# Kernel optimization log

Measured on AMD Instinct MI355X. Metric: run time of the kernel, lower is better.

## Reference

```python
import jax, jax.numpy as jnp
import numpy as np

B, E, S = 64, 256, 32        # batch, projection_size (=MHA embed dim), seq_l
H = 16                        # MHA heads
D_FINAL = 10                  # label space
K_CLASSES = D_FINAL * (D_FINAL - 1) // 2 + 1  # 46, header output dim
N_PATIENTS = 8
P_PAIRS = N_PATIENTS * (B // N_PATIENTS) ** 2  # 512 same-patient pairs (static)


def _pair_lookup(D):
    # class id of sorted label pair: (0,0)->0, then (a,b) a<b in lexicographic
    # order, matching torch.unique(rows of triu meshgrid) ordering.
    lut = np.zeros((D, D), np.int32)
    idx = 1
    for a in range(D):
        for b in range(a + 1, D):
            lut[a, b] = idx
            lut[b, a] = idx
            idx += 1
    return lut


def setup_inputs():
    ks = jax.random.split(jax.random.key(0), 10)
    s = 1.0 / np.sqrt(E)
    return {
        "features": jax.random.normal(ks[0], (B, E, S), jnp.float32),
        "labels0": jax.random.randint(ks[1], (B,), 0, D_FINAL, jnp.int32),
        "labels1": (jnp.arange(B, dtype=jnp.int32) // (B // N_PATIENTS)),
        "in_proj_w": jax.random.normal(ks[2], (3 * E, E), jnp.float32) * s,
        "in_proj_b": jax.random.normal(ks[3], (3 * E,), jnp.float32) * 0.01,
        "out_proj_w": jax.random.normal(ks[4], (E, E), jnp.float32) * s,
        "out_proj_b": jax.random.normal(ks[5], (E,), jnp.float32) * 0.01,
        "final_w": jax.random.normal(ks[6], (1, S), jnp.float32) * (1.0 / np.sqrt(S)),
        "final_b": jax.random.normal(ks[7], (1,), jnp.float32) * 0.01,
        "header_w": jax.random.normal(ks[8], (K_CLASSES, E), jnp.float32) * s,
        "header_b": jax.random.normal(ks[9], (K_CLASSES,), jnp.float32) * 0.01,
    }


def reference(features, labels0, labels1, in_proj_w, in_proj_b, out_proj_w,
              out_proj_b, final_w, final_b, header_w, header_b):
    # ---- pair selection: (i, j) with same patient id (labels1) ----
    mask = (labels1[:, None] == labels1[None, :]).reshape(-1)  # (B*B,)
    sel = jnp.nonzero(mask, size=P_PAIRS, fill_value=0)[0]      # row-major order
    valid = (jnp.arange(P_PAIRS) < mask.sum()).astype(jnp.float32)
    i_idx, j_idx = sel // B, sel % B                            # (P,), (P,)

    # ---- pair class labels: sorted (l_i, l_j), equal labels -> (0, 0) ----
    a, b = labels0[i_idx], labels0[j_idx]
    eq = a == b
    lo = jnp.where(eq, 0, jnp.minimum(a, b))
    hi = jnp.where(eq, 0, jnp.maximum(a, b))
    lut = jnp.asarray(_pair_lookup(D_FINAL))
    y = lut[lo, hi]                                             # (P,) class ids

    # ---- gather pair features; torch permutes to (2, P, seq_l, C) ----
    q_in = jnp.transpose(features[i_idx], (0, 2, 1))  # (P, S, E) query
    kv_in = jnp.transpose(features[j_idx], (0, 2, 1))  # (P, S, E) key/value

    # ---- MultiheadAttention (eval, dropout off); L = pair axis P, N = S ----
    Wq, Wk, Wv = jnp.split(in_proj_w, 3, axis=0)
    bq, bk, bv = jnp.split(in_proj_b, 3, axis=0)
    hd = E // H
    q = (q_in @ Wq.T + bq).reshape(P_PAIRS, S, H, hd)
    k = (kv_in @ Wk.T + bk).reshape(P_PAIRS, S, H, hd)
    v = (kv_in @ Wv.T + bv).reshape(P_PAIRS, S, H, hd)
    scores = jnp.einsum('lshd,mshd->shlm', q, k) / np.sqrt(hd)  # (S,H,P,P)
    attn = jax.nn.softmax(scores, axis=-1)
    o = jnp.einsum('shlm,mshd->lshd', attn, v).reshape(P_PAIRS, S, E)
    o = o @ out_proj_w.T + out_proj_b                           # (P, S, E)

    # ---- backbone.final: Linear over the seq axis (S -> 1), squeeze ----
    h = jnp.einsum('pse,s->pe', o, final_w[0]) + final_b[0]     # (P, E)
    logits = h @ header_w.T + header_b                          # (P, K)

    # ---- inverse-frequency class weights over selected pairs ----
    counts = jnp.zeros(K_CLASSES, jnp.float32).at[y].add(valid)
    w = jnp.where(counts > 0, 1.0 / jnp.maximum(counts, 1.0), 0.0)

    # ---- weighted cross-entropy (torch semantics: / sum of weights) ----
    nll = -jax.nn.log_softmax(logits, axis=-1)[jnp.arange(P_PAIRS), y]
    wy = w[y] * valid
    loss = jnp.sum(wy * nll) / jnp.sum(wy)
    return loss
```

## Files before the change

### kernel.cpp

```cpp
#include <hip/hip_runtime.h>
#include <math.h>

#define B_ 64
#define E_ 256
#define S_ 32
#define H_ 16
#define P_ 512
#define KC_ 46
#define QKV_N (B_*S_*E_)

#define WS_CM     0
#define WS_WK     256
#define WS_INVDEN 3328
#define WS_C      3392
#define WS_M      3584
#define WS_WT     16384
#define WS_QKV    262144
#define WS_OPART  1835008

__global__ __launch_bounds__(256) void k_prep(
    const float* __restrict__ w, const int* __restrict__ labels0,
    const int* __restrict__ labels1, const float* __restrict__ wout,
    const float* __restrict__ bout, const float* __restrict__ fw,
    const float* __restrict__ fbi, const float* __restrict__ hw,
    const float* __restrict__ hb, float* __restrict__ ws,
    float* __restrict__ out) {
  __shared__ float sm[8192];
  const int bid = blockIdx.x, t = threadIdx.x;
  if (bid < 48) {
    const int r0 = (bid >> 2) * 64, c0 = (bid & 3) * 64;
    float* ts = sm;
#pragma unroll
    for (int p = 0; p < 4; ++p) {
      int r = p*16 + (t >> 4), c4 = t & 15;
      float4 v = *(const float4*)(w + (size_t)(r0+r)*E_ + c0 + c4*4);
      ts[(c4*4+0)*65 + r] = v.x;
      ts[(c4*4+1)*65 + r] = v.y;
      ts[(c4*4+2)*65 + r] = v.z;
      ts[(c4*4+3)*65 + r] = v.w;
    }
    __syncthreads();
    float* WT = ws + WS_WT;
#pragma unroll
    for (int p = 0; p < 4; ++p) {
      int c = p*16 + (t >> 4), r4 = t & 15;
      float4 v = make_float4(ts[c*65 + r4*4], ts[c*65 + r4*4 + 1],
                             ts[c*65 + r4*4 + 2], ts[c*65 + r4*4 + 3]);
      *(float4*)(WT + (size_t)(c0+c)*768 + r0 + r4*4) = v;
    }
  } else if (bid == 48) {
    float* csh = sm;
    float* cls = sm + 64;
    float* wsh = sm + 112;
    float* den = sm + 160;
    float* Wk  = sm + 192;
    int* scan = (int*)(sm + 3200);
    int* l0   = (int*)(sm + 3456);
    int* l1   = (int*)(sm + 3520);
    int* seli = (int*)(sm + 3584);
    int* selj = (int*)(sm + 4096);
    if (t < 64) { l0[t] = labels0[t]; l1[t] = labels1[t]; csh[t] = 0.f; }
    if (t < KC_) cls[t] = 0.f;
    if (t == 0) den[0] = 0.f;
    for (int i = t; i < 2944; i += 256) Wk[i] = 0.f;
    __syncthreads();
    unsigned bits = 0; int c = 0;
    for (int u = 0; u < 16; ++u) {
      int idx = t*16 + u;
      if (l1[idx>>6] == l1[idx&63]) { bits |= 1u<<u; ++c; }
    }
    scan[t] = c; __syncthreads();
    for (int off = 1; off < 256; off <<= 1) {
      int v = (t >= off) ? scan[t-off] : 0;
      __syncthreads();
      scan[t] += v;
      __syncthreads();
    }
    const int total = scan[255];
    int rank = scan[t] - c;
    for (int p = t; p < P_; p += 256)
      if (p >= total) { seli[p] = 0; selj[p] = 0; }
    for (int u = 0; u < 16; ++u) {
      if (bits & (1u<<u)) {
        if (rank < P_) { int idx = t*16+u; seli[rank] = idx>>6; selj[rank] = idx&63; }
        ++rank;
      }
    }
    __syncthreads();
    int ii[2], yy[2]; float vv[2];
#pragma unroll
    for (int r = 0; r < 2; ++r) {
      int p = t + r*256;
      int i = seli[p], j = selj[p];
      atomicAdd(&csh[j], 1.0f);
      int la = l0[i], lb = l0[j];
      int y;
      if (la == lb) y = 0;
      else {
        int lo = la < lb ? la : lb, hi = la < lb ? lb : la;
        y = 1 + lo*9 - (lo*(lo-1))/2 + (hi-lo-1);
      }
      float v = (p < total) ? 1.f : 0.f;
      if (v > 0.f) atomicAdd(&cls[y], 1.f);
      ii[r] = i; yy[r] = y; vv[r] = v;
    }
    __syncthreads();
    if (t < KC_) {
      float cv = cls[t];
      wsh[t] = cv > 0.f ? 1.0f/cv : 0.f;
      if (cv > 0.f) atomicAdd(den, 1.0f);
    }
    __syncthreads();
#pragma unroll
    for (int r = 0; r < 2; ++r)
      if (vv[r] > 0.f) atomicAdd(&Wk[ii[r]*KC_ + yy[r]], wsh[yy[r]]);
    __syncthreads();
    if (t < 64) ws[WS_CM + t] = csh[t];
    for (int i = t; i < 2944; i += 256) ws[WS_WK + i] = Wk[i];
    if (t == 0) ws[WS_INVDEN] = 1.0f / den[0];
  } else if (bid < 95) {
    int k = bid - 49;
    float* hwsh = sm;
    float* redA = sm + 256;
    float* redB = sm + 512;
    hwsh[t] = hw[k*E_ + t];
    __syncthreads();
    float a0 = 0.f;
#pragma unroll 8
    for (int e = 0; e < E_; ++e) a0 = fmaf(hwsh[e], wout[e*E_ + t], a0);
    ws[WS_M + k*E_ + t] = a0;
    redA[t] = hwsh[t];
    redB[t] = hwsh[t]*bout[t];
    __syncthreads();
    for (int off = 128; off > 0; off >>= 1) {
      if (t < off) { redA[t] += redA[t+off]; redB[t] += redB[t+off]; }
      __syncthreads();
    }
    if (t == 0) {
      float sfw = 0.f;
      for (int s = 0; s < S_; ++s) sfw += fw[s];
      ws[WS_C + k] = fbi[0]*redA[0] + sfw*redB[0] + hb[k];
    }
  } else {
    if (t == 0) out[0] = 0.f;
  }
}

__global__ __launch_bounds__(256) void k_proj(
    const float* __restrict__ feat, const float* __restrict__ bias,
    float* __restrict__ ws) {
  const int cc = blockIdx.x, b = blockIdx.y, t = threadIdx.x;
  __shared__ float xs[E_*S_];
  float4* xs4 = (float4*)xs;
  const float4* fb4 = (const float4*)(feat + (size_t)b*(E_*S_));
#pragma unroll
  for (int i = 0; i < 8; ++i) xs4[i*256 + t] = fb4[i*256 + t];
  __syncthreads();
  const int to = t & 31, ts = t >> 5;
  const float4* WT4 = (const float4*)(ws + WS_WT);
  const int wi = cc*32 + to;
  float acc[4][4];
#pragma unroll
  for (int o = 0; o < 4; ++o)
#pragma unroll
    for (int si = 0; si < 4; ++si) acc[o][si] = 0.f;
#pragma unroll 4
  for (int e = 0; e < E_; ++e) {
    float4 wv4 = WT4[e*192 + wi];
    float4 x4  = xs4[e*8 + ts];
    float wv[4] = {wv4.x, wv4.y, wv4.z, wv4.w};
    float xv[4] = {x4.x, x4.y, x4.z, x4.w};
#pragma unroll
    for (int o = 0; o < 4; ++o)
#pragma unroll
      for (int si = 0; si < 4; ++si)
        acc[o][si] = fmaf(wv[o], xv[si], acc[o][si]);
  }
  const int out0 = cc*128 + to*4;
  float4 bb = *(const float4*)(bias + out0);
  const int r = out0 >> 8, e_in = out0 & 255;
  float* dst = ws + WS_QKV + (size_t)r*QKV_N + (size_t)b*(S_*E_) + e_in;
#pragma unroll
  for (int si = 0; si < 4; ++si) {
    int s = ts*4 + si;
    *(float4*)(dst + s*E_) = make_float4(acc[0][si]+bb.x, acc[1][si]+bb.y,
                                         acc[2][si]+bb.z, acc[3][si]+bb.w);
  }
}

__global__ __launch_bounds__(256) void k_attn(
    float* __restrict__ ws, const float* __restrict__ fw) {
  const int s = blockIdx.x >> 4, h = blockIdx.x & 15;
  const int t = threadIdx.x;
  __shared__ float qT[16*68], kT[16*68], vs[64*20];
  __shared__ float sc[64*68], pT[64*68], red[4*64*20], cm[64];
  const float* qkv = ws + WS_QKV;
  const int a = t >> 2, dq = t & 3;
  {
    size_t off = (size_t)a*(S_*E_) + (size_t)s*E_ + h*16 + dq*4;
    float4 q4 = *(const float4*)(qkv + off);
    float4 k4 = *(const float4*)(qkv + QKV_N + off);
    float4 v4 = *(const float4*)(qkv + 2*(size_t)QKV_N + off);
    qT[(dq*4+0)*68 + a] = q4.x; qT[(dq*4+1)*68 + a] = q4.y;
    qT[(dq*4+2)*68 + a] = q4.z; qT[(dq*4+3)*68 + a] = q4.w;
    kT[(dq*4+0)*68 + a] = k4.x; kT[(dq*4+1)*68 + a] = k4.y;
    kT[(dq*4+2)*68 + a] = k4.z; kT[(dq*4+3)*68 + a] = k4.w;
    *(float4*)(vs + a*20 + dq*4) = v4;
  }
  if (t < 64) cm[t] = ws[WS_CM + t];
  __syncthreads();
  const int ta = t & 15, tb = t >> 4;
  float sa[4][4];
#pragma unroll
  for (int r = 0; r < 4; ++r)
#pragma unroll
    for (int c = 0; c < 4; ++c) sa[r][c] = 0.f;
#pragma unroll
  for (int d = 0; d < 16; ++d) {
    float4 qv = *(float4*)(qT + d*68 + ta*4);
    float4 kv = *(float4*)(kT + d*68 + tb*4);
    float qr[4] = {qv.x,qv.y,qv.z,qv.w};
    float kc[4] = {kv.x,kv.y,kv.z,kv.w};
#pragma unroll
    for (int r = 0; r < 4; ++r)
#pragma unroll
      for (int c = 0; c < 4; ++c) sa[r][c] = fmaf(qr[r], kc[c], sa[r][c]);
  }
#pragma unroll
  for (int r = 0; r < 4; ++r)
    *(float4*)(sc + (ta*4+r)*68 + tb*4) =
        make_float4(sa[r][0]*0.25f, sa[r][1]*0.25f, sa[r][2]*0.25f, sa[r][3]*0.25f);
  __syncthreads();
  float pv[16], cmv[16];
#pragma unroll
  for (int i4 = 0; i4 < 4; ++i4) {
    float4 v = *(float4*)(sc + a*68 + dq*16 + i4*4);
    pv[i4*4+0] = v.x; pv[i4*4+1] = v.y; pv[i4*4+2] = v.z; pv[i4*4+3] = v.w;
  }
#pragma unroll
  for (int i = 0; i < 16; ++i) cmv[i] = cm[dq*16 + i];
  float Mx = -1e30f;
#pragma unroll
  for (int i = 0; i < 16; ++i) if (cmv[i] > 0.f) Mx = fmaxf(Mx, pv[i]);
  Mx = fmaxf(Mx, __shfl_xor(Mx, 1));
  Mx = fmaxf(Mx, __shfl_xor(Mx, 2));
  float z = 0.f;
#pragma unroll
  for (int i = 0; i < 16; ++i) {
    float e = (cmv[i] > 0.f) ? cmv[i]*__expf(pv[i]-Mx) : 0.f;
    pv[i] = e; z += e;
  }
  z += __shfl_xor(z, 1);
  z += __shfl_xor(z, 2);
  float rz = 1.0f / z;
#pragma unroll
  for (int i = 0; i < 16; ++i) pT[(dq*16+i)*68 + a] = pv[i]*rz;
  __syncthreads();
  const int g = t >> 6, td = (t >> 4) & 3, ta2 = t & 15;
  float o[4][4];
#pragma unroll
  for (int r = 0; r < 4; ++r)
#pragma unroll
    for (int c = 0; c < 4; ++c) o[r][c] = 0.f;
#pragma unroll
  for (int i = 0; i < 16; ++i) {
    int bb = g*16 + i;
    float4 p4 = *(float4*)(pT + bb*68 + ta2*4);
    float4 v4 = *(float4*)(vs + bb*20 + td*4);
    float pr[4] = {p4.x,p4.y,p4.z,p4.w};
    float vc[4] = {v4.x,v4.y,v4.z,v4.w};
#pragma unroll
    for (int r = 0; r < 4; ++r)
#pragma unroll
      for (int c = 0; c < 4; ++c) o[r][c] = fmaf(pr[r], vc[c], o[r][c]);
  }
#pragma unroll
  for (int r = 0; r < 4; ++r)
    *(float4*)(red + g*1280 + (ta2*4+r)*20 + td*4) =
        make_float4(o[r][0], o[r][1], o[r][2], o[r][3]);
  __syncthreads();
  const float fwS = fw[s];
  float4 osum = make_float4(0.f, 0.f, 0.f, 0.f);
#pragma unroll
  for (int g2 = 0; g2 < 4; ++g2) {
    float4 v = *(float4*)(red + g2*1280 + a*20 + dq*4);
    osum.x += v.x; osum.y += v.y; osum.z += v.z; osum.w += v.w;
  }
  float* dst = ws + WS_OPART + (size_t)s*(H_*B_*16) + h*(B_*16) + a*16 + dq*4;
  *(float4*)dst = make_float4(fwS*osum.x, fwS*osum.y, fwS*osum.z, fwS*osum.w);
}

__global__ __launch_bounds__(256) void k_final(
    const float* __restrict__ ws, float* __restrict__ out) {
  const int aa = blockIdx.x, t = threadIdx.x;
  __shared__ float oh[256], lg[64];
  {
    const float* op = ws + WS_OPART + (t>>4)*(B_*16) + aa*16 + (t&15);
    float acc = 0.f;
#pragma unroll
    for (int s = 0; s < S_; ++s) acc += op[(size_t)s*(H_*B_*16)];
    oh[t] = acc;
  }
  __syncthreads();
  const int k = t >> 2, q = t & 3;
  if (k < KC_) {
    float lv = 0.f;
    const float4* M4 = (const float4*)(ws + WS_M + k*E_ + q*64);
    const float4* o4 = (const float4*)(oh + q*64);
#pragma unroll
    for (int j = 0; j < 16; ++j) {
      float4 m = M4[j], o = o4[j];
      lv = fmaf(m.x, o.x, lv); lv = fmaf(m.y, o.y, lv);
      lv = fmaf(m.z, o.z, lv); lv = fmaf(m.w, o.w, lv);
    }
    lv += __shfl_xor(lv, 1);
    lv += __shfl_xor(lv, 2);
    if (q == 0) lg[k] = lv + ws[WS_C + k];
  }
  __syncthreads();
  if (t < 64) {
    float x = (t < KC_) ? lg[t] : -1e30f;
    float Mx = x;
#pragma unroll
    for (int off = 1; off < 64; off <<= 1) Mx = fmaxf(Mx, __shfl_xor(Mx, off));
    float z = (t < KC_) ? __expf(x - Mx) : 0.f;
#pragma unroll
    for (int off = 1; off < 64; off <<= 1) z += __shfl_xor(z, off);
    float lse = Mx + __logf(z);
    float term = (t < KC_) ? ws[WS_WK + aa*KC_ + t] * (lse - x) : 0.f;
#pragma unroll
    for (int off = 1; off < 64; off <<= 1) term += __shfl_xor(term, off);
    if (t == 0) atomicAdd(out, term * ws[WS_INVDEN]);
  }
}

extern "C" void kernel_launch(void* const* d_in, const int* in_sizes, int n_in,
                              void* d_out, int out_size, void* d_ws, size_t ws_size,
                              hipStream_t stream) {
  const float* feat    = (const float*)d_in[0];
  const int*   labels0 = (const int*)d_in[1];
  const int*   labels1 = (const int*)d_in[2];
  const float* ipw     = (const float*)d_in[3];
  const float* ipb     = (const float*)d_in[4];
  const float* opw     = (const float*)d_in[5];
  const float* opb     = (const float*)d_in[6];
  const float* fw      = (const float*)d_in[7];
  const float* fbi     = (const float*)d_in[8];
  const float* hw      = (const float*)d_in[9];
  const float* hb      = (const float*)d_in[10];
  float* out = (float*)d_out;
  float* ws  = (float*)d_ws;

  k_prep<<<96, 256, 0, stream>>>(ipw, labels0, labels1, opw, opb, fw, fbi,
                                 hw, hb, ws, out);
  k_proj<<<dim3(6, 64), 256, 0, stream>>>(feat, ipb, ws);
  k_attn<<<512, 256, 0, stream>>>(ws, fw);
  k_final<<<64, 256, 0, stream>>>(ws, out);
}
```

Baseline: 126.9 us.

## Fuse all four stages into one cooperative kernel with grid-wide syncs

Replaces the four separate kernel launches (prep, projection, attention, final) with a single cooperative kernel of 512 blocks that separates stages with grid.sync(). The QKV projection is remapped so each block handles one batch row and 96 outputs, with each thread computing 12 outputs for one sequence position. The attention stage reuses the score buffer for probabilities and drops the cross-group reduction buffer by having each thread accumulate over all 64 keys. This removes launch gaps and inter-kernel drain, at the cost of grid-barrier overhead and a cooperative launch that requires all 512 blocks to be co-resident, with each block holding 32 KB of shared memory.

```diff
diff --git a/kernel.cpp b/kernel.cpp
--- a/kernel.cpp
+++ b/kernel.cpp
@@ -1,5 +1,8 @@
 #include <hip/hip_runtime.h>
+#include <hip/hip_cooperative_groups.h>
 #include <math.h>
+
+namespace cg = cooperative_groups;
 
 #define B_ 64
 #define E_ 256
@@ -18,22 +21,24 @@
 #define WS_QKV    262144
 #define WS_OPART  1835008
 
-__global__ __launch_bounds__(256) void k_prep(
-    const float* __restrict__ w, const int* __restrict__ labels0,
-    const int* __restrict__ labels1, const float* __restrict__ wout,
-    const float* __restrict__ bout, const float* __restrict__ fw,
+__global__ __launch_bounds__(256) void k_fused(
+    const float* __restrict__ feat, const int* __restrict__ labels0,
+    const int* __restrict__ labels1, const float* __restrict__ ipw,
+    const float* __restrict__ ipb, const float* __restrict__ opw,
+    const float* __restrict__ opb, const float* __restrict__ fw,
     const float* __restrict__ fbi, const float* __restrict__ hw,
-    const float* __restrict__ hb, float* __restrict__ ws,
-    float* __restrict__ out) {
+    const float* __restrict__ hb, float* ws, float* out) {
   __shared__ float sm[8192];
+  cg::grid_group grid = cg::this_grid();
   const int bid = blockIdx.x, t = threadIdx.x;
+
   if (bid < 48) {
     const int r0 = (bid >> 2) * 64, c0 = (bid & 3) * 64;
     float* ts = sm;
 #pragma unroll
     for (int p = 0; p < 4; ++p) {
       int r = p*16 + (t >> 4), c4 = t & 15;
-      float4 v = *(const float4*)(w + (size_t)(r0+r)*E_ + c0 + c4*4);
+      float4 v = *(const float4*)(ipw + (size_t)(r0+r)*E_ + c0 + c4*4);
       ts[(c4*4+0)*65 + r] = v.x;
       ts[(c4*4+1)*65 + r] = v.y;
       ts[(c4*4+2)*65 + r] = v.z;
@@ -127,10 +132,10 @@
     __syncthreads();
     float a0 = 0.f;
 #pragma unroll 8
-    for (int e = 0; e < E_; ++e) a0 = fmaf(hwsh[e], wout[e*E_ + t], a0);
+    for (int e = 0; e < E_; ++e) a0 = fmaf(hwsh[e], opw[e*E_ + t], a0);
     ws[WS_M + k*E_ + t] = a0;
     redA[t] = hwsh[t];
-    redB[t] = hwsh[t]*bout[t];
+    redB[t] = hwsh[t]*opb[t];
     __syncthreads();
     for (int off = 128; off > 0; off >>= 1) {
       if (t < off) { redA[t] += redA[t+off]; redB[t] += redB[t+off]; }
@@ -141,196 +146,192 @@
       for (int s = 0; s < S_; ++s) sfw += fw[s];
       ws[WS_C + k] = fbi[0]*redA[0] + sfw*redB[0] + hb[k];
     }
-  } else {
+  } else if (bid == 95) {
     if (t == 0) out[0] = 0.f;
   }
-}
-
-__global__ __launch_bounds__(256) void k_proj(
-    const float* __restrict__ feat, const float* __restrict__ bias,
-    float* __restrict__ ws) {
-  const int cc = blockIdx.x, b = blockIdx.y, t = threadIdx.x;
-  __shared__ float xs[E_*S_];
-  float4* xs4 = (float4*)xs;
-  const float4* fb4 = (const float4*)(feat + (size_t)b*(E_*S_));
-#pragma unroll
-  for (int i = 0; i < 8; ++i) xs4[i*256 + t] = fb4[i*256 + t];
-  __syncthreads();
-  const int to = t & 31, ts = t >> 5;
-  const float4* WT4 = (const float4*)(ws + WS_WT);
-  const int wi = cc*32 + to;
-  float acc[4][4];
-#pragma unroll
-  for (int o = 0; o < 4; ++o)
-#pragma unroll
-    for (int si = 0; si < 4; ++si) acc[o][si] = 0.f;
+  grid.sync();
+
+  {
+    const int b = bid >> 3, oc = bid & 7;
+    const float4* fb4 = (const float4*)(feat + (size_t)b*(E_*S_));
+    float4* xs4 = (float4*)sm;
+#pragma unroll
+    for (int i = 0; i < 8; ++i) xs4[i*256 + t] = fb4[i*256 + t];
+    __syncthreads();
+    const int s = t & 31, to8 = t >> 5;
+    const int out0 = oc*96 + to8*12;
+    const float4* WT4 = (const float4*)(ws + WS_WT);
+    const int wbase = out0 >> 2;
+    float acc[12];
+#pragma unroll
+    for (int i = 0; i < 12; ++i) acc[i] = 0.f;
 #pragma unroll 4
-  for (int e = 0; e < E_; ++e) {
-    float4 wv4 = WT4[e*192 + wi];
-    float4 x4  = xs4[e*8 + ts];
-    float wv[4] = {wv4.x, wv4.y, wv4.z, wv4.w};
-    float xv[4] = {x4.x, x4.y, x4.z, x4.w};
-#pragma unroll
-    for (int o = 0; o < 4; ++o)
-#pragma unroll
-      for (int si = 0; si < 4; ++si)
-        acc[o][si] = fmaf(wv[o], xv[si], acc[o][si]);
+    for (int e = 0; e < E_; ++e) {
+      float xv = sm[e*32 + s];
+      float4 w0 = WT4[e*192 + wbase];
+      float4 w1 = WT4[e*192 + wbase + 1];
+      float4 w2 = WT4[e*192 + wbase + 2];
+      acc[0] = fmaf(w0.x, xv, acc[0]);  acc[1] = fmaf(w0.y, xv, acc[1]);
+      acc[2] = fmaf(w0.z, xv, acc[2]);  acc[3] = fmaf(w0.w, xv, acc[3]);
+      acc[4] = fmaf(w1.x, xv, acc[4]);  acc[5] = fmaf(w1.y, xv, acc[5]);
+      acc[6] = fmaf(w1.z, xv, acc[6]);  acc[7] = fmaf(w1.w, xv, acc[7]);
+      acc[8] = fmaf(w2.x, xv, acc[8]);  acc[9] = fmaf(w2.y, xv, acc[9]);
+      acc[10] = fmaf(w2.z, xv, acc[10]); acc[11] = fmaf(w2.w, xv, acc[11]);
+    }
+#pragma unroll
+    for (int g = 0; g < 3; ++g) {
+      int og = out0 + g*4;
+      float4 bb = *(const float4*)(ipb + og);
+      int r = og >> 8, e_in = og & 255;
+      float* dst = ws + WS_QKV + (size_t)r*QKV_N + (size_t)b*(S_*E_) + s*E_ + e_in;
+      *(float4*)dst = make_float4(acc[g*4+0]+bb.x, acc[g*4+1]+bb.y,
+                                  acc[g*4+2]+bb.z, acc[g*4+3]+bb.w);
+    }
   }
-  const int out0 = cc*128 + to*4;
-  float4 bb = *(const float4*)(bias + out0);
-  const int r = out0 >> 8, e_in = out0 & 255;
-  float* dst = ws + WS_QKV + (size_t)r*QKV_N + (size_t)b*(S_*E_) + e_in;
-#pragma unroll
-  for (int si = 0; si < 4; ++si) {
-    int s = ts*4 + si;
-    *(float4*)(dst + s*E_) = make_float4(acc[0][si]+bb.x, acc[1][si]+bb.y,
-                                         acc[2][si]+bb.z, acc[3][si]+bb.w);
+  grid.sync();
+
+  {
+    float* qT = sm;
+    float* kT = sm + 1088;
+    float* vs = sm + 2176;
+    float* sc = sm + 3456;
+    float* cm = sm + 7808;
+    const int s = bid >> 4, h = bid & 15;
+    const int a = t >> 2, dq = t & 3;
+    const float* qkv = ws + WS_QKV;
+    {
+      size_t off = (size_t)a*(S_*E_) + (size_t)s*E_ + h*16 + dq*4;
+      float4 q4 = *(const float4*)(qkv + off);
+      float4 k4 = *(const float4*)(qkv + QKV_N + off);
+      float4 v4 = *(const float4*)(qkv + 2*(size_t)QKV_N + off);
+      qT[(dq*4+0)*68 + a] = q4.x; qT[(dq*4+1)*68 + a] = q4.y;
+      qT[(dq*4+2)*68 + a] = q4.z; qT[(dq*4+3)*68 + a] = q4.w;
+      kT[(dq*4+0)*68 + a] = k4.x; kT[(dq*4+1)*68 + a] = k4.y;
+      kT[(dq*4+2)*68 + a] = k4.z; kT[(dq*4+3)*68 + a] = k4.w;
+      *(float4*)(vs + a*20 + dq*4) = v4;
+    }
+    if (t < 64) cm[t] = ws[WS_CM + t];
+    __syncthreads();
+    {
+      const int ta = t & 15, tb = t >> 4;
+      float sa[4][4];
+#pragma unroll
+      for (int r = 0; r < 4; ++r)
+#pragma unroll
+        for (int c = 0; c < 4; ++c) sa[r][c] = 0.f;
+#pragma unroll
+      for (int d = 0; d < 16; ++d) {
+        float4 qv = *(float4*)(qT + d*68 + ta*4);
+        float4 kv = *(float4*)(kT + d*68 + tb*4);
+        float qr[4] = {qv.x,qv.y,qv.z,qv.w};
+        float kc[4] = {kv.x,kv.y,kv.z,kv.w};
+#pragma unroll
+        for (int r = 0; r < 4; ++r)
+#pragma unroll
+          for (int c = 0; c < 4; ++c) sa[r][c] = fmaf(qr[r], kc[c], sa[r][c]);
+      }
+#pragma unroll
+      for (int r = 0; r < 4; ++r)
+        *(float4*)(sc + (ta*4+r)*68 + tb*4) =
+            make_float4(sa[r][0]*0.25f, sa[r][1]*0.25f,
+                        sa[r][2]*0.25f, sa[r][3]*0.25f);
+    }
+    __syncthreads();
+    {
+      float pv[16], cmv[16];
+#pragma unroll
+      for (int i4 = 0; i4 < 4; ++i4) {
+        float4 v = *(float4*)(sc + a*68 + dq*16 + i4*4);
+        pv[i4*4+0] = v.x; pv[i4*4+1] = v.y; pv[i4*4+2] = v.z; pv[i4*4+3] = v.w;
+      }
+#pragma unroll
+      for (int i = 0; i < 16; ++i) cmv[i] = cm[dq*16 + i];
+      float Mx = -1e30f;
+#pragma unroll
+      for (int i = 0; i < 16; ++i) if (cmv[i] > 0.f) Mx = fmaxf(Mx, pv[i]);
+      Mx = fmaxf(Mx, __shfl_xor(Mx, 1));
+      Mx = fmaxf(Mx, __shfl_xor(Mx, 2));
+      float z = 0.f;
+#pragma unroll
+      for (int i = 0; i < 16; ++i) {
+        float e = (cmv[i] > 0.f) ? cmv[i]*__expf(pv[i]-Mx) : 0.f;
+        pv[i] = e; z += e;
+      }
+      z += __shfl_xor(z, 1);
+      z += __shfl_xor(z, 2);
+      float rz = 1.0f / z;
+#pragma unroll
+      for (int i4 = 0; i4 < 4; ++i4)
+        *(float4*)(sc + a*68 + dq*16 + i4*4) =
+            make_float4(pv[i4*4+0]*rz, pv[i4*4+1]*rz,
+                        pv[i4*4+2]*rz, pv[i4*4+3]*rz);
+    }
+    __syncthreads();
+    {
+      const int g = t >> 6, l = t & 63;
+      const int ar = g*16 + (l >> 2), d4 = (l & 3)*4;
+      float o0 = 0.f, o1 = 0.f, o2 = 0.f, o3 = 0.f;
+#pragma unroll 4
+      for (int b4 = 0; b4 < 64; b4 += 4) {
+        float4 p4 = *(float4*)(sc + ar*68 + b4);
+        float4 va = *(float4*)(vs + (b4+0)*20 + d4);
+        float4 vb = *(float4*)(vs + (b4+1)*20 + d4);
+        float4 vc = *(float4*)(vs + (b4+2)*20 + d4);
+        float4 vd = *(float4*)(vs + (b4+3)*20 + d4);
+        o0 = fmaf(p4.x, va.x, fmaf(p4.y, vb.x, fmaf(p4.z, vc.x, fmaf(p4.w, vd.x, o0))));
+        o1 = fmaf(p4.x, va.y, fmaf(p4.y, vb.y, fmaf(p4.z, vc.y, fmaf(p4.w, vd.y, o1))));
+        o2 = fmaf(p4.x, va.z, fmaf(p4.y, vb.z, fmaf(p4.z, vc.z, fmaf(p4.w, vd.z, o2))));
+        o3 = fmaf(p4.x, va.w, fmaf(p4.y, vb.w, fmaf(p4.z, vc.w, fmaf(p4.w, vd.w, o3))));
+      }
+      const float fwS = fw[s];
+      float* dst = ws + WS_OPART + (size_t)s*(H_*B_*16) + h*(B_*16) + t*4;
+      *(float4*)dst = make_float4(fwS*o0, fwS*o1, fwS*o2, fwS*o3);
+    }
   }
-}
-
-__global__ __launch_bounds__(256) void k_attn(
-    float* __restrict__ ws, const float* __restrict__ fw) {
-  const int s = blockIdx.x >> 4, h = blockIdx.x & 15;
-  const int t = threadIdx.x;
-  __shared__ float qT[16*68], kT[16*68], vs[64*20];
-  __shared__ float sc[64*68], pT[64*68], red[4*64*20], cm[64];
-  const float* qkv = ws + WS_QKV;
-  const int a = t >> 2, dq = t & 3;
-  {
-    size_t off = (size_t)a*(S_*E_) + (size_t)s*E_ + h*16 + dq*4;
-    float4 q4 = *(const float4*)(qkv + off);
-    float4 k4 = *(const float4*)(qkv + QKV_N + off);
-    float4 v4 = *(const float4*)(qkv + 2*(size_t)QKV_N + off);
-    qT[(dq*4+0)*68 + a] = q4.x; qT[(dq*4+1)*68 + a] = q4.y;
-    qT[(dq*4+2)*68 + a] = q4.z; qT[(dq*4+3)*68 + a] = q4.w;
-    kT[(dq*4+0)*68 + a] = k4.x; kT[(dq*4+1)*68 + a] = k4.y;
-    kT[(dq*4+2)*68 + a] = k4.z; kT[(dq*4+3)*68 + a] = k4.w;
-    *(float4*)(vs + a*20 + dq*4) = v4;
-  }
-  if (t < 64) cm[t] = ws[WS_CM + t];
-  __syncthreads();
-  const int ta = t & 15, tb = t >> 4;
-  float sa[4][4];
-#pragma unroll
-  for (int r = 0; r < 4; ++r)
-#pragma unroll
-    for (int c = 0; c < 4; ++c) sa[r][c] = 0.f;
-#pragma unroll
-  for (int d = 0; d < 16; ++d) {
-    float4 qv = *(float4*)(qT + d*68 + ta*4);
-    float4 kv = *(float4*)(kT + d*68 + tb*4);
-    float qr[4] = {qv.x,qv.y,qv.z,qv.w};
-    float kc[4] = {kv.x,kv.y,kv.z,kv.w};
-#pragma unroll
-    for (int r = 0; r < 4; ++r)
-#pragma unroll
-      for (int c = 0; c < 4; ++c) sa[r][c] = fmaf(qr[r], kc[c], sa[r][c]);
-  }
-#pragma unroll
-  for (int r = 0; r < 4; ++r)
-    *(float4*)(sc + (ta*4+r)*68 + tb*4) =
-        make_float4(sa[r][0]*0.25f, sa[r][1]*0.25f, sa[r][2]*0.25f, sa[r][3]*0.25f);
-  __syncthreads();
-  float pv[16], cmv[16];
-#pragma unroll
-  for (int i4 = 0; i4 < 4; ++i4) {
-    float4 v = *(float4*)(sc + a*68 + dq*16 + i4*4);
-    pv[i4*4+0] = v.x; pv[i4*4+1] = v.y; pv[i4*4+2] = v.z; pv[i4*4+3] = v.w;
-  }
-#pragma unroll
-  for (int i = 0; i < 16; ++i) cmv[i] = cm[dq*16 + i];
-  float Mx = -1e30f;
-#pragma unroll
-  for (int i = 0; i < 16; ++i) if (cmv[i] > 0.f) Mx = fmaxf(Mx, pv[i]);
-  Mx = fmaxf(Mx, __shfl_xor(Mx, 1));
-  Mx = fmaxf(Mx, __shfl_xor(Mx, 2));
-  float z = 0.f;
-#pragma unroll
-  for (int i = 0; i < 16; ++i) {
-    float e = (cmv[i] > 0.f) ? cmv[i]*__expf(pv[i]-Mx) : 0.f;
-    pv[i] = e; z += e;
-  }
-  z += __shfl_xor(z, 1);
-  z += __shfl_xor(z, 2);
-  float rz = 1.0f / z;
-#pragma unroll
-  for (int i = 0; i < 16; ++i) pT[(dq*16+i)*68 + a] = pv[i]*rz;
-  __syncthreads();
-  const int g = t >> 6, td = (t >> 4) & 3, ta2 = t & 15;
-  float o[4][4];
-#pragma unroll
-  for (int r = 0; r < 4; ++r)
-#pragma unroll
-    for (int c = 0; c < 4; ++c) o[r][c] = 0.f;
-#pragma unroll
-  for (int i = 0; i < 16; ++i) {
-    int bb = g*16 + i;
-    float4 p4 = *(float4*)(pT + bb*68 + ta2*4);
-    float4 v4 = *(float4*)(vs + bb*20 + td*4);
-    float pr[4] = {p4.x,p4.y,p4.z,p4.w};
-    float vc[4] = {v4.x,v4.y,v4.z,v4.w};
-#pragma unroll
-    for (int r = 0; r < 4; ++r)
-#pragma unroll
-      for (int c = 0; c < 4; ++c) o[r][c] = fmaf(pr[r], vc[c], o[r][c]);
-  }
-#pragma unroll
-  for (int r = 0; r < 4; ++r)
-    *(float4*)(red + g*1280 + (ta2*4+r)*20 + td*4) =
-        make_float4(o[r][0], o[r][1], o[r][2], o[r][3]);
-  __syncthreads();
-  const float fwS = fw[s];
-  float4 osum = make_float4(0.f, 0.f, 0.f, 0.f);
-#pragma unroll
-  for (int g2 = 0; g2 < 4; ++g2) {
-    float4 v = *(float4*)(red + g2*1280 + a*20 + dq*4);
-    osum.x += v.x; osum.y += v.y; osum.z += v.z; osum.w += v.w;
-  }
-  float* dst = ws + WS_OPART + (size_t)s*(H_*B_*16) + h*(B_*16) + a*16 + dq*4;
-  *(float4*)dst = make_float4(fwS*osum.x, fwS*osum.y, fwS*osum.z, fwS*osum.w);
-}
-
-__global__ __launch_bounds__(256) void k_final(
-    const float* __restrict__ ws, float* __restrict__ out) {
-  const int aa = blockIdx.x, t = threadIdx.x;
-  __shared__ float oh[256], lg[64];
-  {
-    const float* op = ws + WS_OPART + (t>>4)*(B_*16) + aa*16 + (t&15);
-    float acc = 0.f;
-#pragma unroll
-    for (int s = 0; s < S_; ++s) acc += op[(size_t)s*(H_*B_*16)];
-    oh[t] = acc;
-  }
-  __syncthreads();
-  const int k = t >> 2, q = t & 3;
-  if (k < KC_) {
-    float lv = 0.f;
-    const float4* M4 = (const float4*)(ws + WS_M + k*E_ + q*64);
-    const float4* o4 = (const float4*)(oh + q*64);
-#pragma unroll
-    for (int j = 0; j < 16; ++j) {
-      float4 m = M4[j], o = o4[j];
-      lv = fmaf(m.x, o.x, lv); lv = fmaf(m.y, o.y, lv);
-      lv = fmaf(m.z, o.z, lv); lv = fmaf(m.w, o.w, lv);
-    }
-    lv += __shfl_xor(lv, 1);
-    lv += __shfl_xor(lv, 2);
-    if (q == 0) lg[k] = lv + ws[WS_C + k];
-  }
-  __syncthreads();
-  if (t < 64) {
-    float x = (t < KC_) ? lg[t] : -1e30f;
-    float Mx = x;
-#pragma unroll
-    for (int off = 1; off < 64; off <<= 1) Mx = fmaxf(Mx, __shfl_xor(Mx, off));
-    float z = (t < KC_) ? __expf(x - Mx) : 0.f;
-#pragma unroll
-    for (int off = 1; off < 64; off <<= 1) z += __shfl_xor(z, off);
-    float lse = Mx + __logf(z);
-    float term = (t < KC_) ? ws[WS_WK + aa*KC_ + t] * (lse - x) : 0.f;
-#pragma unroll
-    for (int off = 1; off < 64; off <<= 1) term += __shfl_xor(term, off);
-    if (t == 0) atomicAdd(out, term * ws[WS_INVDEN]);
+  grid.sync();
+
+  if (bid < 64) {
+    const int aa = bid;
+    float* oh = sm;
+    float* lg = sm + 256;
+    {
+      const float* op = ws + WS_OPART + (t>>4)*(B_*16) + aa*16 + (t&15);
+      float acc = 0.f;
+#pragma unroll
+      for (int s = 0; s < S_; ++s) acc += op[(size_t)s*(H_*B_*16)];
+      oh[t] = acc;
+    }
+    __syncthreads();
+    const int k = t >> 2, q = t & 3;
+    if (k < KC_) {
+      float lv = 0.f;
+      const float4* M4 = (const float4*)(ws + WS_M + k*E_ + q*64);
+      const float4* o4 = (const float4*)(oh + q*64);
+#pragma unroll
+      for (int j = 0; j < 16; ++j) {
+        float4 m = M4[j], o = o4[j];
+        lv = fmaf(m.x, o.x, lv); lv = fmaf(m.y, o.y, lv);
+        lv = fmaf(m.z, o.z, lv); lv = fmaf(m.w, o.w, lv);
+      }
+      lv += __shfl_xor(lv, 1);
+      lv += __shfl_xor(lv, 2);
+      if (q == 0) lg[k] = lv + ws[WS_C + k];
+    }
+    __syncthreads();
+    if (t < 64) {
+      float x = (t < KC_) ? lg[t] : -1e30f;
+      float Mx = x;
+#pragma unroll
+      for (int off = 1; off < 64; off <<= 1) Mx = fmaxf(Mx, __shfl_xor(Mx, off));
+      float z = (t < KC_) ? __expf(x - Mx) : 0.f;
+#pragma unroll
+      for (int off = 1; off < 64; off <<= 1) z += __shfl_xor(z, off);
+      float lse = Mx + __logf(z);
+      float term = (t < KC_) ? ws[WS_WK + aa*KC_ + t] * (lse - x) : 0.f;
+#pragma unroll
+      for (int off = 1; off < 64; off <<= 1) term += __shfl_xor(term, off);
+      if (t == 0) atomicAdd(out, term * ws[WS_INVDEN]);
+    }
   }
 }
 
@@ -351,9 +352,8 @@
   float* out = (float*)d_out;
   float* ws  = (float*)d_ws;
 
-  k_prep<<<96, 256, 0, stream>>>(ipw, labels0, labels1, opw, opb, fw, fbi,
-                                 hw, hb, ws, out);
-  k_proj<<<dim3(6, 64), 256, 0, stream>>>(feat, ipb, ws);
-  k_attn<<<512, 256, 0, stream>>>(ws, fw);
-  k_final<<<64, 256, 0, stream>>>(ws, out);
+  void* args[] = {(void*)&feat, (void*)&labels0, (void*)&labels1, (void*)&ipw,
+                  (void*)&ipb, (void*)&opw, (void*)&opb, (void*)&fw,
+                  (void*)&fbi, (void*)&hw, (void*)&hb, (void*)&ws, (void*)&out};
+  hipLaunchCooperativeKernel((void*)k_fused, dim3(512), dim3(256), args, 0, stream);
 }
```

Measured after the change: 335.1 us. 2.64x slower.
